# Performance work log

Hardware: AMD Instinct MI355X
Metric: run time of the kernel (lower is better)

The kernel has to match this reference:

```python
import jax, jax.numpy as jnp
import numpy as np

B, C, H, W = 8, 256, 64, 64
CK = 64  # C // k with k=4


def setup_inputs() -> dict:
    key = jax.random.key(0)
    ks = jax.random.split(key, 5)
    s = 1.0 / np.sqrt(C)
    return {
        "x": jax.random.normal(ks[0], (B, C, H, W), dtype=jnp.float32),
        "wq": jax.random.normal(ks[1], (CK, C), dtype=jnp.float32) * s,
        "bq": jnp.zeros((CK,), dtype=jnp.float32),
        "wk": jax.random.normal(ks[2], (CK, C), dtype=jnp.float32) * s,
        "bk": jnp.zeros((CK,), dtype=jnp.float32),
        "wv": jax.random.normal(ks[3], (C, C), dtype=jnp.float32) * s,
        "bv": jnp.zeros((C,), dtype=jnp.float32),
        "wg": jax.random.normal(ks[4], (C, C), dtype=jnp.float32) * s,
        "bg": jnp.zeros((C,), dtype=jnp.float32),
    }


def reference(x, wq, bq, wk, bk, wv, bv, wg, bg):
    b, c, h, w = x.shape
    n = h * w
    xf = x.reshape(b, c, n)  # [B, C, N]
    # 1x1 convs are channel-wise matmuls
    q = jnp.einsum('oc,bcn->bon', wq, xf) + bq[None, :, None]  # [B, Ck, N]
    k = jnp.einsum('oc,bcn->bon', wk, xf) + bk[None, :, None]  # [B, Ck, N]
    v = jnp.einsum('oc,bcn->bon', wv, xf) + bv[None, :, None]  # [B, C, N]
    # energy[b,i,j] = q[b,:,i] . k[b,:,j]
    energy = jnp.einsum('bci,bcj->bij', q, k)  # [B, N, N]
    energy = jax.nn.elu(energy) / n
    out = jnp.einsum('bcn,bnj->bcj', v, energy).reshape(b, c, h, w)
    out = jnp.einsum('oc,bchw->bohw', wg, out) + bg[None, :, None, None]
    return out
```

## Files before the change

### kernel.cpp

```cpp
#include <hip/hip_runtime.h>
#include <math.h>

#define BATCH 8
#define CH    256
#define NPIX  4096
#define CKDIM 64

typedef __attribute__((ext_vector_type(8))) short short8;
typedef __attribute__((ext_vector_type(4))) float f32x4;

#define MFMA16x16(a, b, c) __builtin_amdgcn_mfma_f32_16x16x32_bf16((a), (b), (c), 0, 0, 0)

__device__ __forceinline__ unsigned short f2bf(float f) {
    union { float f; unsigned int u; } v; v.f = f;
    unsigned int u = v.u;
    u += 0x7fffu + ((u >> 16) & 1u);
    return (unsigned short)(u >> 16);
}

__global__ void prep_kernel(const float* __restrict__ wq, const float* __restrict__ bq,
                            const float* __restrict__ wk, const float* __restrict__ bk,
                            const float* __restrict__ wv, const float* __restrict__ bv,
                            const float* __restrict__ wg,
                            unsigned short* __restrict__ W_all, float* __restrict__ bias_all) {
    int o = blockIdx.x;
    int c = threadIdx.x;
    if (o < 64) {
        W_all[o * CH + c] = f2bf(wq[o * CH + c]);
        if (c == 0) bias_all[o] = bq[o];
    } else if (o < 128) {
        int oo = o - 64;
        W_all[o * CH + c] = f2bf(wk[oo * CH + c]);
        if (c == 0) bias_all[o] = bk[oo];
    } else {
        int oo = o - 128;
        float acc = 0.f;
        for (int m = 0; m < CH; ++m)
            acc += wg[oo * CH + m] * wv[m * CH + c];
        W_all[o * CH + c] = f2bf(acc);
        if (c == 0) {
            float b = 0.f;
            for (int m = 0; m < CH; ++m) b += wg[oo * CH + m] * bv[m];
            bias_all[o] = b;
        }
    }
}

__global__ void xpose_kernel(const float* __restrict__ x, unsigned short* __restrict__ xt) {
    __shared__ float Tl[64][65];
    int n0 = blockIdx.x * 64;
    int c0 = blockIdx.y * 64;
    int b  = blockIdx.z;
    int tid = threadIdx.x;

#pragma unroll
    for (int r = 0; r < 4; ++r) {
        int f  = r * 256 + tid;
        int c  = f >> 4;
        int n4 = f & 15;
        float4 v = *(const float4*)(x + ((size_t)b * CH + c0 + c) * NPIX + n0 + n4 * 4);
        Tl[n4 * 4 + 0][c] = v.x;
        Tl[n4 * 4 + 1][c] = v.y;
        Tl[n4 * 4 + 2][c] = v.z;
        Tl[n4 * 4 + 3][c] = v.w;
    }
    __syncthreads();
#pragma unroll
    for (int r = 0; r < 2; ++r) {
        int f    = r * 256 + tid;
        int nrow = f >> 3;
        int c8   = f & 7;
        unsigned int pk[4];
#pragma unroll
        for (int p = 0; p < 4; ++p) {
            unsigned int lo = f2bf(Tl[nrow][c8 * 8 + p * 2 + 0]);
            unsigned int hi = f2bf(Tl[nrow][c8 * 8 + p * 2 + 1]);
            pk[p] = lo | (hi << 16);
        }
        *(uint4*)(xt + ((size_t)b * NPIX + n0 + nrow) * CH + c0 + c8 * 8) = *(uint4*)pk;
    }
}

__global__ void qkv_mfma(const unsigned short* __restrict__ xt,
                         const unsigned short* __restrict__ W_all,
                         const float* __restrict__ bias_all,
                         unsigned short* __restrict__ qk, unsigned short* __restrict__ vp) {
    __shared__ __align__(16) unsigned short Xl[64][264];

    int n0   = blockIdx.x * 64;
    int b    = blockIdx.y;
    int tid  = threadIdx.x;
    int lane = tid & 63;
    int w    = tid >> 6;
    int col  = lane & 15;
    int quad = lane >> 4;

#pragma unroll
    for (int r = 0; r < 8; ++r) {
        int f   = r * 256 + tid;
        int row = f >> 5;
        int c8  = f & 31;
        *(uint4*)&Xl[row][c8 * 8] = *(const uint4*)(xt + ((size_t)b * NPIX + n0 + row) * CH + c8 * 8);
    }
    __syncthreads();

#pragma unroll
    for (int og = 0; og < 6; ++og) {
        int o0 = og * 64;
        const unsigned short* Arow = W_all + (size_t)(o0 + w * 16 + col) * CH + quad * 8;

        f32x4 acc[4];
#pragma unroll
        for (int t = 0; t < 4; ++t) acc[t] = (f32x4){0.f, 0.f, 0.f, 0.f};

#pragma unroll
        for (int kc = 0; kc < 8; ++kc) {
            short8 a = *(const short8*)(Arow + kc * 32);
#pragma unroll
            for (int nt = 0; nt < 4; ++nt) {
                short8 bb = *(const short8*)&Xl[nt * 16 + col][kc * 32 + quad * 8];
                acc[nt] = MFMA16x16(a, bb, acc[nt]);
            }
        }

        float4 bias = *(const float4*)(bias_all + o0 + w * 16 + quad * 4);
        float bs[4] = {bias.x, bias.y, bias.z, bias.w};

        if (og < 2) {
#pragma unroll
            for (int nt = 0; nt < 4; ++nt) {
                int n = n0 + nt * 16 + col;
                unsigned int pk[2];
#pragma unroll
                for (int p = 0; p < 2; ++p) {
                    unsigned int lo = f2bf(acc[nt][p * 2 + 0] + bs[p * 2 + 0]);
                    unsigned int hi = f2bf(acc[nt][p * 2 + 1] + bs[p * 2 + 1]);
                    pk[p] = lo | (hi << 16);
                }
                *(uint2*)(qk + ((size_t)b * NPIX + n) * 128 + o0 + w * 16 + quad * 4) = *(uint2*)pk;
            }
        } else {
#pragma unroll
            for (int nt = 0; nt < 4; ++nt) {
                int n = n0 + nt * 16 + col;
#pragma unroll
                for (int r = 0; r < 4; ++r) {
                    int oo = o0 - 128 + w * 16 + quad * 4 + r;
                    vp[((size_t)b * CH + oo) * NPIX + n] = f2bf(acc[nt][r] + bs[r]);
                }
            }
        }
    }
}

#define LPK 72
__global__ __launch_bounds__(512, 4)
void attn_v6(const unsigned short* __restrict__ qk,
             const unsigned short* __restrict__ vp,
             const float* __restrict__ bg, float* __restrict__ out) {
    __shared__ __align__(16) unsigned short Qt[64][LPK];
    __shared__ __align__(16) unsigned short St[64][LPK];

    int lin  = blockIdx.y * gridDim.x + blockIdx.x;
    int b    = lin & 7;
    int j0   = (lin >> 3) * 64;
    int tid  = threadIdx.x;
    int lane = tid & 63;
    int w    = tid >> 6;
    int col  = lane & 15;
    int quad = lane >> 4;

    int tjA = w & 3;
    int tiP = (w >> 2) * 2;

    short8 bK[2];
#pragma unroll
    for (int ks = 0; ks < 2; ++ks)
        bK[ks] = *(const short8*)(qk + ((size_t)b * NPIX + j0 + tjA * 16 + col) * 128 + 64 + ks * 32 + quad * 8);

    f32x4 acc[2][4];
#pragma unroll
    for (int ot = 0; ot < 2; ++ot)
#pragma unroll
        for (int tj = 0; tj < 4; ++tj) acc[ot][tj] = (f32x4){0.f, 0.f, 0.f, 0.f};

    int qrow = tid >> 3, q8 = tid & 7;
    const unsigned short* Qsrc = qk + ((size_t)b * NPIX + qrow) * 128 + q8 * 8;
    const unsigned short* Vsrc[2];
#pragma unroll
    for (int ot = 0; ot < 2; ++ot)
        Vsrc[ot] = vp + ((size_t)b * CH + (w * 2 + ot) * 16 + col) * NPIX + quad * 8;

    uint4 qr = *(const uint4*)Qsrc;
    short8 vb[2][2];
#pragma unroll
    for (int ot = 0; ot < 2; ++ot)
#pragma unroll
        for (int ks = 0; ks < 2; ++ks)
            vb[ot][ks] = *(const short8*)(Vsrc[ot] + ks * 32);

    const float invN = 1.f / (float)NPIX;

    for (int i0 = 0; i0 < NPIX; i0 += 64) {
        *(uint4*)&Qt[qrow][q8 * 8] = qr;

        int inext = (i0 + 64) & (NPIX - 1);
        uint4 qr_n = *(const uint4*)(Qsrc + (size_t)inext * 128);
        short8 vb_n[2][2];
#pragma unroll
        for (int ot = 0; ot < 2; ++ot)
#pragma unroll
            for (int ks = 0; ks < 2; ++ks)
                vb_n[ot][ks] = *(const short8*)(Vsrc[ot] + inext + ks * 32);

        __syncthreads();

#pragma unroll
        for (int t = 0; t < 2; ++t) {
            int ti = tiP + t;
            short8 a0 = *(const short8*)&Qt[ti * 16 + col][quad * 8];
            short8 a1 = *(const short8*)&Qt[ti * 16 + col][32 + quad * 8];
            f32x4 s = (f32x4){0.f, 0.f, 0.f, 0.f};
            s = MFMA16x16(a0, bK[0], s);
            s = MFMA16x16(a1, bK[1], s);
            unsigned int pk2[2];
#pragma unroll
            for (int pp = 0; pp < 2; ++pp) {
                float e0 = s[pp * 2 + 0];
                float e1 = s[pp * 2 + 1];
                float g0 = __expf(e0) - 1.f;
                float g1 = __expf(e1) - 1.f;
                e0 = (e0 > 0.f) ? e0 : g0;
                e1 = (e1 > 0.f) ? e1 : g1;
                e0 *= invN;
                e1 *= invN;
                unsigned int rpk;
                asm("v_cvt_pk_bf16_f32 %0, %1, %2" : "=v"(rpk) : "v"(e0), "v"(e1));
                pk2[pp] = rpk;
            }
            *(uint2*)&St[tjA * 16 + col][ti * 16 + quad * 4] = *(uint2*)pk2;
        }
        __syncthreads();

#pragma unroll
        for (int ks = 0; ks < 2; ++ks) {
            short8 sb[4];
#pragma unroll
            for (int tj = 0; tj < 4; ++tj)
                sb[tj] = *(const short8*)&St[tj * 16 + col][ks * 32 + quad * 8];
            __builtin_amdgcn_s_setprio(1);
#pragma unroll
            for (int ot = 0; ot < 2; ++ot)
#pragma unroll
                for (int tj = 0; tj < 4; ++tj)
                    acc[ot][tj] = MFMA16x16(sb[tj], vb[ot][ks], acc[ot][tj]);
            __builtin_amdgcn_s_setprio(0);
        }

        qr = qr_n;
#pragma unroll
        for (int ot = 0; ot < 2; ++ot)
#pragma unroll
            for (int ks = 0; ks < 2; ++ks)
                vb[ot][ks] = vb_n[ot][ks];
    }

#pragma unroll
    for (int ot = 0; ot < 2; ++ot) {
        int o = (w * 2 + ot) * 16 + col;
        float bgv = bg[o];
#pragma unroll
        for (int tj = 0; tj < 4; ++tj) {
            int j = j0 + tj * 16 + quad * 4;
            float4 st;
            st.x = acc[ot][tj][0] + bgv;
            st.y = acc[ot][tj][1] + bgv;
            st.z = acc[ot][tj][2] + bgv;
            st.w = acc[ot][tj][3] + bgv;
            *(float4*)&out[((size_t)b * CH + o) * NPIX + j] = st;
        }
    }
}

extern "C" void kernel_launch(void* const* d_in, const int* in_sizes, int n_in,
                              void* d_out, int out_size, void* d_ws, size_t ws_size,
                              hipStream_t stream) {
    const float* x  = (const float*)d_in[0];
    const float* wq = (const float*)d_in[1];
    const float* bq = (const float*)d_in[2];
    const float* wk = (const float*)d_in[3];
    const float* bk = (const float*)d_in[4];
    const float* wv = (const float*)d_in[5];
    const float* bv = (const float*)d_in[6];
    const float* wg = (const float*)d_in[7];
    const float* bg = (const float*)d_in[8];
    float* out = (float*)d_out;

    unsigned short* W_all = (unsigned short*)d_ws;
    float* bias_all = (float*)(W_all + 384 * 256);
    unsigned short* xt = (unsigned short*)(bias_all + 384);
    unsigned short* qk = xt + (size_t)BATCH * NPIX * CH;
    unsigned short* vp = qk + (size_t)BATCH * NPIX * 128;

    prep_kernel<<<dim3(384), dim3(256), 0, stream>>>(wq, bq, wk, bk, wv, bv, wg, W_all, bias_all);
    xpose_kernel<<<dim3(NPIX / 64, CH / 64, BATCH), dim3(256), 0, stream>>>(x, xt);
    qkv_mfma<<<dim3(NPIX / 64, BATCH), dim3(256), 0, stream>>>(xt, W_all, bias_all, qk, vp);
    attn_v6<<<dim3(NPIX / 64, BATCH), dim3(512), 0, stream>>>(qk, vp, bg, out);
}
```

Before: 266.0 us.

## Double-buffer energy tile and load Q fragments directly from global memory

Drops the shared-memory Q staging tile and has each wave load its Q MFMA fragments straight from global memory. The energy/ELU tile for the next step is computed into a second shared buffer while the current tile feeds the V MFMAs, which cuts the barriers per iteration from two to one. The cost is extra LDS for the second buffer, more registers live across the loop, and uncoalesced or redundant global Q loads across waves.

```diff
diff --git a/kernel.cpp b/kernel.cpp
--- a/kernel.cpp
+++ b/kernel.cpp
@@ -155,11 +155,10 @@
 
 #define LPK 72
 __global__ __launch_bounds__(512, 4)
-void attn_v6(const unsigned short* __restrict__ qk,
+void attn_v7(const unsigned short* __restrict__ qk,
              const unsigned short* __restrict__ vp,
              const float* __restrict__ bg, float* __restrict__ out) {
-    __shared__ __align__(16) unsigned short Qt[64][LPK];
-    __shared__ __align__(16) unsigned short St[64][LPK];
+    __shared__ __align__(16) unsigned short St[2][64][LPK];
 
     int lin  = blockIdx.y * gridDim.x + blockIdx.x;
     int b    = lin & 7;
@@ -184,42 +183,27 @@
 #pragma unroll
         for (int tj = 0; tj < 4; ++tj) acc[ot][tj] = (f32x4){0.f, 0.f, 0.f, 0.f};
 
-    int qrow = tid >> 3, q8 = tid & 7;
-    const unsigned short* Qsrc = qk + ((size_t)b * NPIX + qrow) * 128 + q8 * 8;
-    const unsigned short* Vsrc[2];
+    const unsigned short* Qb = qk + ((size_t)b * NPIX + col) * 128 + quad * 8;
+    const unsigned short* Vs[2];
 #pragma unroll
     for (int ot = 0; ot < 2; ++ot)
-        Vsrc[ot] = vp + ((size_t)b * CH + (w * 2 + ot) * 16 + col) * NPIX + quad * 8;
-
-    uint4 qr = *(const uint4*)Qsrc;
+        Vs[ot] = vp + ((size_t)b * CH + (w * 2 + ot) * 16 + col) * NPIX + quad * 8;
+
+    const float invN = 1.f / (float)NPIX;
+
     short8 vb[2][2];
 #pragma unroll
     for (int ot = 0; ot < 2; ++ot)
 #pragma unroll
         for (int ks = 0; ks < 2; ++ks)
-            vb[ot][ks] = *(const short8*)(Vsrc[ot] + ks * 32);
-
-    const float invN = 1.f / (float)NPIX;
-
-    for (int i0 = 0; i0 < NPIX; i0 += 64) {
-        *(uint4*)&Qt[qrow][q8 * 8] = qr;
-
-        int inext = (i0 + 64) & (NPIX - 1);
-        uint4 qr_n = *(const uint4*)(Qsrc + (size_t)inext * 128);
-        short8 vb_n[2][2];
-#pragma unroll
-        for (int ot = 0; ot < 2; ++ot)
-#pragma unroll
-            for (int ks = 0; ks < 2; ++ks)
-                vb_n[ot][ks] = *(const short8*)(Vsrc[ot] + inext + ks * 32);
-
-        __syncthreads();
-
-#pragma unroll
-        for (int t = 0; t < 2; ++t) {
-            int ti = tiP + t;
-            short8 a0 = *(const short8*)&Qt[ti * 16 + col][quad * 8];
-            short8 a1 = *(const short8*)&Qt[ti * 16 + col][32 + quad * 8];
+            vb[ot][ks] = *(const short8*)(Vs[ot] + ks * 32);
+
+    {
+#pragma unroll
+        for (int t2 = 0; t2 < 2; ++t2) {
+            int ti = tiP + t2;
+            short8 a0 = *(const short8*)(Qb + (size_t)(ti * 16) * 128);
+            short8 a1 = *(const short8*)(Qb + (size_t)(ti * 16) * 128 + 32);
             f32x4 s = (f32x4){0.f, 0.f, 0.f, 0.f};
             s = MFMA16x16(a0, bK[0], s);
             s = MFMA16x16(a1, bK[1], s);
@@ -238,16 +222,38 @@
                 asm("v_cvt_pk_bf16_f32 %0, %1, %2" : "=v"(rpk) : "v"(e0), "v"(e1));
                 pk2[pp] = rpk;
             }
-            *(uint2*)&St[tjA * 16 + col][ti * 16 + quad * 4] = *(uint2*)pk2;
-        }
+            *(uint2*)&St[0][tjA * 16 + col][ti * 16 + quad * 4] = *(uint2*)pk2;
+        }
+    }
+
+    for (int it = 0; it < NPIX / 64; ++it) {
+        int cur  = it & 1;
+        int more = (it + 1) < (NPIX / 64);
+        size_t inext = (size_t)(it + 1) * 64;
+
         __syncthreads();
+
+        short8 qa_n[2][2], vb_n[2][2];
+        if (more) {
+#pragma unroll
+            for (int t2 = 0; t2 < 2; ++t2) {
+                const unsigned short* qrow = Qb + (inext + (size_t)(tiP + t2) * 16) * 128;
+                qa_n[t2][0] = *(const short8*)(qrow);
+                qa_n[t2][1] = *(const short8*)(qrow + 32);
+            }
+#pragma unroll
+            for (int ot = 0; ot < 2; ++ot)
+#pragma unroll
+                for (int ks = 0; ks < 2; ++ks)
+                    vb_n[ot][ks] = *(const short8*)(Vs[ot] + inext + ks * 32);
+        }
 
 #pragma unroll
         for (int ks = 0; ks < 2; ++ks) {
             short8 sb[4];
 #pragma unroll
             for (int tj = 0; tj < 4; ++tj)
-                sb[tj] = *(const short8*)&St[tj * 16 + col][ks * 32 + quad * 8];
+                sb[tj] = *(const short8*)&St[cur][tj * 16 + col][ks * 32 + quad * 8];
             __builtin_amdgcn_s_setprio(1);
 #pragma unroll
             for (int ot = 0; ot < 2; ++ot)
@@ -257,12 +263,36 @@
             __builtin_amdgcn_s_setprio(0);
         }
 
-        qr = qr_n;
-#pragma unroll
-        for (int ot = 0; ot < 2; ++ot)
-#pragma unroll
-            for (int ks = 0; ks < 2; ++ks)
-                vb[ot][ks] = vb_n[ot][ks];
+        if (more) {
+#pragma unroll
+            for (int t2 = 0; t2 < 2; ++t2) {
+                int ti = tiP + t2;
+                f32x4 s = (f32x4){0.f, 0.f, 0.f, 0.f};
+                s = MFMA16x16(qa_n[t2][0], bK[0], s);
+                s = MFMA16x16(qa_n[t2][1], bK[1], s);
+                unsigned int pk2[2];
+#pragma unroll
+                for (int pp = 0; pp < 2; ++pp) {
+                    float e0 = s[pp * 2 + 0];
+                    float e1 = s[pp * 2 + 1];
+                    float g0 = __expf(e0) - 1.f;
+                    float g1 = __expf(e1) - 1.f;
+                    e0 = (e0 > 0.f) ? e0 : g0;
+                    e1 = (e1 > 0.f) ? e1 : g1;
+                    e0 *= invN;
+                    e1 *= invN;
+                    unsigned int rpk;
+                    asm("v_cvt_pk_bf16_f32 %0, %1, %2" : "=v"(rpk) : "v"(e0), "v"(e1));
+                    pk2[pp] = rpk;
+                }
+                *(uint2*)&St[cur ^ 1][tjA * 16 + col][ti * 16 + quad * 4] = *(uint2*)pk2;
+            }
+#pragma unroll
+            for (int ot = 0; ot < 2; ++ot)
+#pragma unroll
+                for (int ks = 0; ks < 2; ++ks)
+                    vb[ot][ks] = vb_n[ot][ks];
+        }
     }
 
 #pragma unroll
@@ -305,5 +335,5 @@
     prep_kernel<<<dim3(384), dim3(256), 0, stream>>>(wq, bq, wk, bk, wv, bv, wg, W_all, bias_all);
     xpose_kernel<<<dim3(NPIX / 64, CH / 64, BATCH), dim3(256), 0, stream>>>(x, xt);
     qkv_mfma<<<dim3(NPIX / 64, BATCH), dim3(256), 0, stream>>>(xt, W_all, bias_all, qk, vp);
-    attn_v6<<<dim3(NPIX / 64, BATCH), dim3(512), 0, stream>>>(qk, vp, bg, out);
-}
+    attn_v7<<<dim3(NPIX / 64, BATCH), dim3(512), 0, stream>>>(qk, vp, bg, out);
+}
```

Result: slower. 378.3 us (+42.2%).

## Retile attention kernel to 32-column blocks with 4 waves and in-loop V loads

Applied to the files above, without the earlier changes.

The attention kernel now handles 32 output columns per block with 256 threads, and each wave covers 64 output channels instead of 32. This doubles the grid to 1024 blocks, which should fill the CUs better, but every Q tile is now loaded and run through the energy MFMA twice as often overall. V fragments are loaded inside the loop after the barrier rather than prefetched a step ahead, which can expose global load latency. The prep kernel also caches the wg row in shared memory and splits its dot product into four accumulators.

```diff
diff --git a/kernel.cpp b/kernel.cpp
--- a/kernel.cpp
+++ b/kernel.cpp
@@ -33,14 +33,22 @@
         W_all[o * CH + c] = f2bf(wk[oo * CH + c]);
         if (c == 0) bias_all[o] = bk[oo];
     } else {
+        __shared__ float wgr[CH];
         int oo = o - 128;
-        float acc = 0.f;
-        for (int m = 0; m < CH; ++m)
-            acc += wg[oo * CH + m] * wv[m * CH + c];
-        W_all[o * CH + c] = f2bf(acc);
+        wgr[c] = wg[oo * CH + c];
+        __syncthreads();
+        float a0 = 0.f, a1 = 0.f, a2 = 0.f, a3 = 0.f;
+#pragma unroll 4
+        for (int m = 0; m < CH; m += 4) {
+            a0 += wgr[m + 0] * wv[(m + 0) * CH + c];
+            a1 += wgr[m + 1] * wv[(m + 1) * CH + c];
+            a2 += wgr[m + 2] * wv[(m + 2) * CH + c];
+            a3 += wgr[m + 3] * wv[(m + 3) * CH + c];
+        }
+        W_all[o * CH + c] = f2bf((a0 + a1) + (a2 + a3));
         if (c == 0) {
             float b = 0.f;
-            for (int m = 0; m < CH; ++m) b += wg[oo * CH + m] * bv[m];
+            for (int m = 0; m < CH; ++m) b += wgr[m] * bv[m];
             bias_all[o] = b;
         }
     }
@@ -154,70 +162,69 @@
 }
 
 #define LPK 72
-__global__ __launch_bounds__(512, 4)
-void attn_v6(const unsigned short* __restrict__ qk,
+__global__ __launch_bounds__(256, 4)
+void attn_v8(const unsigned short* __restrict__ qk,
              const unsigned short* __restrict__ vp,
              const float* __restrict__ bg, float* __restrict__ out) {
     __shared__ __align__(16) unsigned short Qt[64][LPK];
-    __shared__ __align__(16) unsigned short St[64][LPK];
-
-    int lin  = blockIdx.y * gridDim.x + blockIdx.x;
+    __shared__ __align__(16) unsigned short St[32][LPK];
+
+    int lin  = blockIdx.x;
     int b    = lin & 7;
-    int j0   = (lin >> 3) * 64;
+    int j0   = (lin >> 3) * 32;
     int tid  = threadIdx.x;
     int lane = tid & 63;
     int w    = tid >> 6;
     int col  = lane & 15;
     int quad = lane >> 4;
 
-    int tjA = w & 3;
-    int tiP = (w >> 2) * 2;
+    int tjA = w >> 1;
+    int tiP = (w & 1) * 2;
 
     short8 bK[2];
 #pragma unroll
     for (int ks = 0; ks < 2; ++ks)
         bK[ks] = *(const short8*)(qk + ((size_t)b * NPIX + j0 + tjA * 16 + col) * 128 + 64 + ks * 32 + quad * 8);
 
-    f32x4 acc[2][4];
-#pragma unroll
-    for (int ot = 0; ot < 2; ++ot)
-#pragma unroll
-        for (int tj = 0; tj < 4; ++tj) acc[ot][tj] = (f32x4){0.f, 0.f, 0.f, 0.f};
-
-    int qrow = tid >> 3, q8 = tid & 7;
-    const unsigned short* Qsrc = qk + ((size_t)b * NPIX + qrow) * 128 + q8 * 8;
-    const unsigned short* Vsrc[2];
-#pragma unroll
-    for (int ot = 0; ot < 2; ++ot)
-        Vsrc[ot] = vp + ((size_t)b * CH + (w * 2 + ot) * 16 + col) * NPIX + quad * 8;
-
-    uint4 qr = *(const uint4*)Qsrc;
-    short8 vb[2][2];
-#pragma unroll
-    for (int ot = 0; ot < 2; ++ot)
-#pragma unroll
-        for (int ks = 0; ks < 2; ++ks)
-            vb[ot][ks] = *(const short8*)(Vsrc[ot] + ks * 32);
+    f32x4 acc[4][2];
+#pragma unroll
+    for (int ot = 0; ot < 4; ++ot)
+#pragma unroll
+        for (int tj = 0; tj < 2; ++tj) acc[ot][tj] = (f32x4){0.f, 0.f, 0.f, 0.f};
+
+    int srow = tid >> 3, sq8 = tid & 7;
+    const unsigned short* Qsrc = qk + ((size_t)b * NPIX + srow) * 128 + sq8 * 8;
+
+    const unsigned short* Vs[4];
+#pragma unroll
+    for (int ot = 0; ot < 4; ++ot)
+        Vs[ot] = vp + ((size_t)b * CH + (w * 4 + ot) * 16 + col) * NPIX + quad * 8;
 
     const float invN = 1.f / (float)NPIX;
 
+    uint4 qr0 = *(const uint4*)Qsrc;
+    uint4 qr1 = *(const uint4*)(Qsrc + 32 * 128);
+
     for (int i0 = 0; i0 < NPIX; i0 += 64) {
-        *(uint4*)&Qt[qrow][q8 * 8] = qr;
-
-        int inext = (i0 + 64) & (NPIX - 1);
-        uint4 qr_n = *(const uint4*)(Qsrc + (size_t)inext * 128);
-        short8 vb_n[2][2];
-#pragma unroll
-        for (int ot = 0; ot < 2; ++ot)
+        *(uint4*)&Qt[srow][sq8 * 8]      = qr0;
+        *(uint4*)&Qt[srow + 32][sq8 * 8] = qr1;
+
+        size_t inext = (size_t)((i0 + 64) & (NPIX - 1));
+        uint4 qr0_n = *(const uint4*)(Qsrc + inext * 128);
+        uint4 qr1_n = *(const uint4*)(Qsrc + (inext + 32) * 128);
+
+        __syncthreads();
+
+        short8 vb[4][2];
+#pragma unroll
+        for (int ot = 0; ot < 4; ++ot)
 #pragma unroll
             for (int ks = 0; ks < 2; ++ks)
-                vb_n[ot][ks] = *(const short8*)(Vsrc[ot] + inext + ks * 32);
-
-        __syncthreads();
-
-#pragma unroll
-        for (int t = 0; t < 2; ++t) {
-            int ti = tiP + t;
+                vb[ot][ks] = *(const short8*)(Vs[ot] + i0 + ks * 32);
+
+#pragma unroll
+        for (int t2 = 0; t2 < 2; ++t2) {
+            int ti = tiP + t2;
             short8 a0 = *(const short8*)&Qt[ti * 16 + col][quad * 8];
             short8 a1 = *(const short8*)&Qt[ti * 16 + col][32 + quad * 8];
             f32x4 s = (f32x4){0.f, 0.f, 0.f, 0.f};
@@ -244,33 +251,29 @@
 
 #pragma unroll
         for (int ks = 0; ks < 2; ++ks) {
-            short8 sb[4];
-#pragma unroll
-            for (int tj = 0; tj < 4; ++tj)
+            short8 sb[2];
+#pragma unroll
+            for (int tj = 0; tj < 2; ++tj)
                 sb[tj] = *(const short8*)&St[tj * 16 + col][ks * 32 + quad * 8];
             __builtin_amdgcn_s_setprio(1);
 #pragma unroll
-            for (int ot = 0; ot < 2; ++ot)
-#pragma unroll
-                for (int tj = 0; tj < 4; ++tj)
+            for (int ot = 0; ot < 4; ++ot)
+#pragma unroll
+                for (int tj = 0; tj < 2; ++tj)
                     acc[ot][tj] = MFMA16x16(sb[tj], vb[ot][ks], acc[ot][tj]);
             __builtin_amdgcn_s_setprio(0);
         }
 
-        qr = qr_n;
-#pragma unroll
-        for (int ot = 0; ot < 2; ++ot)
-#pragma unroll
-            for (int ks = 0; ks < 2; ++ks)
-                vb[ot][ks] = vb_n[ot][ks];
-    }
-
-#pragma unroll
-    for (int ot = 0; ot < 2; ++ot) {
-        int o = (w * 2 + ot) * 16 + col;
+        qr0 = qr0_n;
+        qr1 = qr1_n;
+    }
+
+#pragma unroll
+    for (int ot = 0; ot < 4; ++ot) {
+        int o = (w * 4 + ot) * 16 + col;
         float bgv = bg[o];
 #pragma unroll
-        for (int tj = 0; tj < 4; ++tj) {
+        for (int tj = 0; tj < 2; ++tj) {
             int j = j0 + tj * 16 + quad * 4;
             float4 st;
             st.x = acc[ot][tj][0] + bgv;
@@ -305,5 +308,5 @@
     prep_kernel<<<dim3(384), dim3(256), 0, stream>>>(wq, bq, wk, bk, wv, bv, wg, W_all, bias_all);
     xpose_kernel<<<dim3(NPIX / 64, CH / 64, BATCH), dim3(256), 0, stream>>>(x, xt);
     qkv_mfma<<<dim3(NPIX / 64, BATCH), dim3(256), 0, stream>>>(xt, W_all, bias_all, qk, vp);
-    attn_v6<<<dim3(NPIX / 64, BATCH), dim3(512), 0, stream>>>(qk, vp, bg, out);
-}
+    attn_v8<<<dim3(NPIX / 32 * BATCH), dim3(256), 0, stream>>>(qk, vp, bg, out);
+}
```

After: 380.6 us. 1.43x slower.

## Halve attention j-tile, split QKV projection over grid z, speed up weight prep

Applied to the files above, without the earlier changes.

The attention kernel now covers 32 output columns per block instead of 64, which doubles the grid to 1024 blocks. Each wave now computes a single 16x16 energy tile, and the launch bound is raised to 8 blocks per CU for more occupancy. The QKV projection is split across two z-slices of three output groups each, and the fused wg*wv prep caches the wg row in LDS and uses four accumulators. In exchange, every Q/V tile is streamed twice as often per output, so global and L2 traffic in attention roughly doubles. Each loaded V fragment also feeds fewer MFMAs.

```diff
diff --git a/kernel.cpp b/kernel.cpp
--- a/kernel.cpp
+++ b/kernel.cpp
@@ -33,14 +33,22 @@
         W_all[o * CH + c] = f2bf(wk[oo * CH + c]);
         if (c == 0) bias_all[o] = bk[oo];
     } else {
+        __shared__ float wgr[CH];
         int oo = o - 128;
-        float acc = 0.f;
-        for (int m = 0; m < CH; ++m)
-            acc += wg[oo * CH + m] * wv[m * CH + c];
-        W_all[o * CH + c] = f2bf(acc);
+        wgr[c] = wg[oo * CH + c];
+        __syncthreads();
+        float a0 = 0.f, a1 = 0.f, a2 = 0.f, a3 = 0.f;
+#pragma unroll 4
+        for (int m = 0; m < CH; m += 4) {
+            a0 += wgr[m + 0] * wv[(m + 0) * CH + c];
+            a1 += wgr[m + 1] * wv[(m + 1) * CH + c];
+            a2 += wgr[m + 2] * wv[(m + 2) * CH + c];
+            a3 += wgr[m + 3] * wv[(m + 3) * CH + c];
+        }
+        W_all[o * CH + c] = f2bf((a0 + a1) + (a2 + a3));
         if (c == 0) {
             float b = 0.f;
-            for (int m = 0; m < CH; ++m) b += wg[oo * CH + m] * bv[m];
+            for (int m = 0; m < CH; ++m) b += wgr[m] * bv[m];
             bias_all[o] = b;
         }
     }
@@ -81,14 +89,16 @@
     }
 }
 
-__global__ void qkv_mfma(const unsigned short* __restrict__ xt,
-                         const unsigned short* __restrict__ W_all,
-                         const float* __restrict__ bias_all,
-                         unsigned short* __restrict__ qk, unsigned short* __restrict__ vp) {
+__global__ __launch_bounds__(256, 4)
+void qkv_mfma(const unsigned short* __restrict__ xt,
+              const unsigned short* __restrict__ W_all,
+              const float* __restrict__ bias_all,
+              unsigned short* __restrict__ qk, unsigned short* __restrict__ vp) {
     __shared__ __align__(16) unsigned short Xl[64][264];
 
     int n0   = blockIdx.x * 64;
     int b    = blockIdx.y;
+    int zg   = blockIdx.z;
     int tid  = threadIdx.x;
     int lane = tid & 63;
     int w    = tid >> 6;
@@ -105,7 +115,8 @@
     __syncthreads();
 
 #pragma unroll
-    for (int og = 0; og < 6; ++og) {
+    for (int ogl = 0; ogl < 3; ++ogl) {
+        int og = zg * 3 + ogl;
         int o0 = og * 64;
         const unsigned short* Arow = W_all + (size_t)(o0 + w * 16 + col) * CH + quad * 8;
 
@@ -154,42 +165,42 @@
 }
 
 #define LPK 72
-__global__ __launch_bounds__(512, 4)
-void attn_v6(const unsigned short* __restrict__ qk,
+__global__ __launch_bounds__(512, 8)
+void attn_v9(const unsigned short* __restrict__ qk,
              const unsigned short* __restrict__ vp,
              const float* __restrict__ bg, float* __restrict__ out) {
     __shared__ __align__(16) unsigned short Qt[64][LPK];
-    __shared__ __align__(16) unsigned short St[64][LPK];
-
-    int lin  = blockIdx.y * gridDim.x + blockIdx.x;
+    __shared__ __align__(16) unsigned short St[32][LPK];
+
+    int lin  = blockIdx.x;
     int b    = lin & 7;
-    int j0   = (lin >> 3) * 64;
+    int j0   = (lin >> 3) * 32;
     int tid  = threadIdx.x;
     int lane = tid & 63;
     int w    = tid >> 6;
     int col  = lane & 15;
     int quad = lane >> 4;
 
-    int tjA = w & 3;
-    int tiP = (w >> 2) * 2;
+    int tjA = w & 1;
+    int tiA = w >> 1;
 
     short8 bK[2];
 #pragma unroll
     for (int ks = 0; ks < 2; ++ks)
         bK[ks] = *(const short8*)(qk + ((size_t)b * NPIX + j0 + tjA * 16 + col) * 128 + 64 + ks * 32 + quad * 8);
 
-    f32x4 acc[2][4];
+    f32x4 acc[2][2];
 #pragma unroll
     for (int ot = 0; ot < 2; ++ot)
 #pragma unroll
-        for (int tj = 0; tj < 4; ++tj) acc[ot][tj] = (f32x4){0.f, 0.f, 0.f, 0.f};
+        for (int tj = 0; tj < 2; ++tj) acc[ot][tj] = (f32x4){0.f, 0.f, 0.f, 0.f};
 
     int qrow = tid >> 3, q8 = tid & 7;
     const unsigned short* Qsrc = qk + ((size_t)b * NPIX + qrow) * 128 + q8 * 8;
-    const unsigned short* Vsrc[2];
+    const unsigned short* Vs[2];
 #pragma unroll
     for (int ot = 0; ot < 2; ++ot)
-        Vsrc[ot] = vp + ((size_t)b * CH + (w * 2 + ot) * 16 + col) * NPIX + quad * 8;
+        Vs[ot] = vp + ((size_t)b * CH + (w * 2 + ot) * 16 + col) * NPIX + quad * 8;
 
     uint4 qr = *(const uint4*)Qsrc;
     short8 vb[2][2];
@@ -197,7 +208,7 @@
     for (int ot = 0; ot < 2; ++ot)
 #pragma unroll
         for (int ks = 0; ks < 2; ++ks)
-            vb[ot][ks] = *(const short8*)(Vsrc[ot] + ks * 32);
+            vb[ot][ks] = *(const short8*)(Vs[ot] + ks * 32);
 
     const float invN = 1.f / (float)NPIX;
 
@@ -211,15 +222,13 @@
         for (int ot = 0; ot < 2; ++ot)
 #pragma unroll
             for (int ks = 0; ks < 2; ++ks)
-                vb_n[ot][ks] = *(const short8*)(Vsrc[ot] + inext + ks * 32);
+                vb_n[ot][ks] = *(const short8*)(Vs[ot] + inext + ks * 32);
 
         __syncthreads();
 
-#pragma unroll
-        for (int t = 0; t < 2; ++t) {
-            int ti = tiP + t;
-            short8 a0 = *(const short8*)&Qt[ti * 16 + col][quad * 8];
-            short8 a1 = *(const short8*)&Qt[ti * 16 + col][32 + quad * 8];
+        {
+            short8 a0 = *(const short8*)&Qt[tiA * 16 + col][quad * 8];
+            short8 a1 = *(const short8*)&Qt[tiA * 16 + col][32 + quad * 8];
             f32x4 s = (f32x4){0.f, 0.f, 0.f, 0.f};
             s = MFMA16x16(a0, bK[0], s);
             s = MFMA16x16(a1, bK[1], s);
@@ -238,21 +247,21 @@
                 asm("v_cvt_pk_bf16_f32 %0, %1, %2" : "=v"(rpk) : "v"(e0), "v"(e1));
                 pk2[pp] = rpk;
             }
-            *(uint2*)&St[tjA * 16 + col][ti * 16 + quad * 4] = *(uint2*)pk2;
+            *(uint2*)&St[tjA * 16 + col][tiA * 16 + quad * 4] = *(uint2*)pk2;
         }
         __syncthreads();
 
 #pragma unroll
         for (int ks = 0; ks < 2; ++ks) {
-            short8 sb[4];
-#pragma unroll
-            for (int tj = 0; tj < 4; ++tj)
+            short8 sb[2];
+#pragma unroll
+            for (int tj = 0; tj < 2; ++tj)
                 sb[tj] = *(const short8*)&St[tj * 16 + col][ks * 32 + quad * 8];
             __builtin_amdgcn_s_setprio(1);
 #pragma unroll
             for (int ot = 0; ot < 2; ++ot)
 #pragma unroll
-                for (int tj = 0; tj < 4; ++tj)
+                for (int tj = 0; tj < 2; ++tj)
                     acc[ot][tj] = MFMA16x16(sb[tj], vb[ot][ks], acc[ot][tj]);
             __builtin_amdgcn_s_setprio(0);
         }
@@ -270,7 +279,7 @@
         int o = (w * 2 + ot) * 16 + col;
         float bgv = bg[o];
 #pragma unroll
-        for (int tj = 0; tj < 4; ++tj) {
+        for (int tj = 0; tj < 2; ++tj) {
             int j = j0 + tj * 16 + quad * 4;
             float4 st;
             st.x = acc[ot][tj][0] + bgv;
@@ -304,6 +313,6 @@
 
     prep_kernel<<<dim3(384), dim3(256), 0, stream>>>(wq, bq, wk, bk, wv, bv, wg, W_all, bias_all);
     xpose_kernel<<<dim3(NPIX / 64, CH / 64, BATCH), dim3(256), 0, stream>>>(x, xt);
-    qkv_mfma<<<dim3(NPIX / 64, BATCH), dim3(256), 0, stream>>>(xt, W_all, bias_all, qk, vp);
-    attn_v6<<<dim3(NPIX / 64, BATCH), dim3(512), 0, stream>>>(qk, vp, bg, out);
-}
+    qkv_mfma<<<dim3(NPIX / 64, BATCH, 2), dim3(256), 0, stream>>>(xt, W_all, bias_all, qk, vp);
+    attn_v9<<<dim3(NPIX / 32 * BATCH), dim3(512), 0, stream>>>(qk, vp, bg, out);
+}
```

Result: slower. 752.1 us (+182.7%).
